# Kernel tuning notes

Hardware: AMD Instinct MI355X
Metric: run time of the kernel (lower is better)

Reference implementation:

```python
import jax, jax.numpy as jnp
import numpy as np

N = 50000
E = 800000
FEAT, COND, HID, LAT = 64, 32, 64, 32


def gcn_conv(x, W, b, src, dst, n):
    xw = x @ W  # [N, out]
    deg = jnp.zeros((n,), xw.dtype).at[dst].add(1.0) + 1.0  # in-degree + self loop
    dinv = jax.lax.rsqrt(deg)
    coef = dinv[src] * dinv[dst]  # [E]
    msg = xw[src] * coef[:, None]  # gather + scale
    agg = jax.ops.segment_sum(msg, dst, num_segments=n)
    agg = agg + xw * (1.0 / deg)[:, None]  # self-loop contribution
    return agg + b


def setup_inputs() -> dict:
    key = jax.random.key(0)
    ks = jax.random.split(key, 12)
    s = 0.05
    return {
        "feature": jax.random.normal(ks[0], (N, FEAT), jnp.float32),
        "condition": jax.random.normal(ks[1], (N, COND), jnp.float32),
        "edge_index": jax.random.randint(ks[2], (2, E), 0, N, jnp.int64),
        "enc_i2h_W": jax.random.normal(ks[3], (FEAT + COND, HID), jnp.float32) * s,
        "enc_i2h_b": jnp.zeros((HID,), jnp.float32),
        "enc_mean_W": jax.random.normal(ks[4], (HID, LAT), jnp.float32) * s,
        "enc_mean_b": jnp.zeros((LAT,), jnp.float32),
        "enc_logvar_W": jax.random.normal(ks[5], (HID, LAT), jnp.float32) * s,
        "enc_logvar_b": jnp.zeros((LAT,), jnp.float32),
        "dec_i2h_W": jax.random.normal(ks[6], (LAT + COND, HID), jnp.float32) * s,
        "dec_i2h_b": jnp.zeros((HID,), jnp.float32),
        "dec_out_W": jax.random.normal(ks[7], (HID, FEAT), jnp.float32) * s,
        "dec_out_b": jnp.zeros((FEAT,), jnp.float32),
    }


def reference(feature, condition, edge_index,
              enc_i2h_W, enc_i2h_b, enc_mean_W, enc_mean_b,
              enc_logvar_W, enc_logvar_b,
              dec_i2h_W, dec_i2h_b, dec_out_W, dec_out_b):
    src, dst = edge_index[0], edge_index[1]
    n = feature.shape[0]
    # encoder
    x = jnp.concatenate([feature, condition], axis=1)
    h = jax.nn.relu(gcn_conv(x, enc_i2h_W, enc_i2h_b, src, dst, n))
    mean = gcn_conv(h, enc_mean_W, enc_mean_b, src, dst, n)
    logvar = gcn_conv(h, enc_logvar_W, enc_logvar_b, src, dst, n)
    noise = jax.random.normal(jax.random.key(42), logvar.shape, logvar.dtype)
    z = noise * jnp.exp(0.5 * logvar) + mean
    # decoder
    xd = jnp.concatenate([z, condition], axis=1)
    hd = jax.nn.relu(gcn_conv(xd, dec_i2h_W, dec_i2h_b, src, dst, n))
    out = gcn_conv(hd, dec_out_W, dec_out_b, src, dst, n)
    return (z, mean, logvar, out)
```

## Files before the change

### kernel.cpp

```cpp
#include <hip/hip_runtime.h>
#include <hip/hip_bf16.h>
#include <hip/hip_fp16.h>
#include <math.h>

typedef _Float16 f16;
typedef __attribute__((ext_vector_type(8))) _Float16 f16x8;
typedef __attribute__((ext_vector_type(4))) float f32x4;


static __device__ __forceinline__ unsigned rotl32(unsigned x, int d) {
  return (x << d) | (x >> (32 - d));
}

static __device__ __forceinline__ void threefry_0_42(unsigned& x0, unsigned& x1) {
  const unsigned ks0 = 0u, ks1 = 42u, ks2 = 0u ^ 42u ^ 0x1BD11BDAu;
  x0 += ks0; x1 += ks1;
#define TF_R(r) { x0 += x1; x1 = rotl32(x1, (r)); x1 ^= x0; }
  TF_R(13) TF_R(15) TF_R(26) TF_R(6)
  x0 += ks1; x1 += ks2 + 1u;
  TF_R(17) TF_R(29) TF_R(16) TF_R(24)
  x0 += ks2; x1 += ks0 + 2u;
  TF_R(13) TF_R(15) TF_R(26) TF_R(6)
  x0 += ks0; x1 += ks1 + 3u;
  TF_R(17) TF_R(29) TF_R(16) TF_R(24)
  x0 += ks1; x1 += ks2 + 4u;
  TF_R(13) TF_R(15) TF_R(26) TF_R(6)
  x0 += ks2; x1 += ks0 + 5u;
#undef TF_R
}

static __device__ __forceinline__ float erfinv_f(float u) {
  float w = -logf((1.0f - u) * (1.0f + u));
  float p;
  if (w < 5.0f) {
    w = w - 2.5f;
    p = 2.81022636e-08f;
    p = fmaf(p, w, 3.43273939e-07f);
    p = fmaf(p, w, -3.5233877e-06f);
    p = fmaf(p, w, -4.39150654e-06f);
    p = fmaf(p, w, 0.00021858087f);
    p = fmaf(p, w, -0.00125372503f);
    p = fmaf(p, w, -0.00417768164f);
    p = fmaf(p, w, 0.246640727f);
    p = fmaf(p, w, 1.50140941f);
  } else {
    w = sqrtf(w) - 3.0f;
    p = -0.000200214257f;
    p = fmaf(p, w, 0.000100950558f);
    p = fmaf(p, w, 0.00134934322f);
    p = fmaf(p, w, -0.00367342844f);
    p = fmaf(p, w, 0.00573950773f);
    p = fmaf(p, w, -0.0076224613f);
    p = fmaf(p, w, 0.00943887047f);
    p = fmaf(p, w, 1.00167406f);
    p = fmaf(p, w, 2.83297682f);
  }
  return p * u;
}

static __device__ __forceinline__ float jax_normal_at(unsigned j) {
  unsigned x0 = 0u, x1 = j;
  threefry_0_42(x0, x1);
  unsigned bits = x0 ^ x1;
  float f = __uint_as_float((bits >> 9) | 0x3f800000u) - 1.0f;
  float u = fmaf(f, 1.99999994f, -0.99999994f);
  return 1.41421356237f * erfinv_f(u);
}


__global__ void degree_i_kernel(const int* __restrict__ dstI, int* __restrict__ cnt, int ne) {
  int e = blockIdx.x * blockDim.x + threadIdx.x;
  if (e < ne) atomicAdd(&cnt[dstI[e]], 1);
}

__global__ __launch_bounds__(256) void bsum_kernel(const int* __restrict__ cnt,
                                                   int* __restrict__ bh, int n) {
  __shared__ int s[256];
  int i = blockIdx.x * 256 + threadIdx.x;
  s[threadIdx.x] = (i < n) ? cnt[i] : 0;
  __syncthreads();
  for (int off = 128; off > 0; off >>= 1) {
    if (threadIdx.x < off) s[threadIdx.x] += s[threadIdx.x + off];
    __syncthreads();
  }
  if (threadIdx.x == 0) bh[blockIdx.x] = s[0];
}

__global__ __launch_bounds__(256) void scanN_kernel(const int* __restrict__ cnt,
                                                    const int* __restrict__ bh,
                                                    int* __restrict__ rowptr,
                                                    float* __restrict__ dinv,
                                                    int* __restrict__ bcur,
                                                    int n, int ne, int nbuck) {
  __shared__ int sb[256];
  __shared__ int sc[256];
  __shared__ int basesh;
  const int t = threadIdx.x;
  const int b = blockIdx.x;
  sb[t] = (t < nbuck) ? bh[t] : 0;
  __syncthreads();
  for (int off = 1; off < 256; off <<= 1) {
    int x = (t >= off) ? sb[t - off] : 0;
    __syncthreads();
    sb[t] += x;
    __syncthreads();
  }
  if (t == 0) basesh = (b > 0) ? sb[b - 1] : 0;
  __syncthreads();

  int i = b * 256 + t;
  int v = (i < n) ? cnt[i] : 0;
  sc[t] = v;
  __syncthreads();
  for (int off = 1; off < 256; off <<= 1) {
    int x = (t >= off) ? sc[t - off] : 0;
    __syncthreads();
    sc[t] += x;
    __syncthreads();
  }
  const int base = basesh;
  if (i < n) {
    rowptr[i] = base + sc[t] - v;
    dinv[i] = 1.0f / sqrtf((float)v + 1.0f);
  }
  if (t == 0) bcur[b] = base;
  if (b == nbuck - 1 && t == 255) rowptr[n] = ne;
}

#define EPB 2048
__global__ __launch_bounds__(256) void fillA_kernel(
    const int* __restrict__ srcI, const int* __restrict__ dstI,
    int* __restrict__ bcur, unsigned* __restrict__ coarse, int ne) {
  __shared__ int hist[256], hpre[256], hcur[256], gbase[256];
  __shared__ unsigned st[EPB];
  const int tid = threadIdx.x;
  const int base = blockIdx.x * EPB;

  hist[tid] = 0; hcur[tid] = 0;
  __syncthreads();

  int s[8], d[8];
#pragma unroll
  for (int k = 0; k < 8; ++k) {
    int e = base + k * 256 + tid;
    if (e < ne) { s[k] = srcI[e]; d[k] = dstI[e]; }
    else        { s[k] = -1;      d[k] = 0; }
  }
#pragma unroll
  for (int k = 0; k < 8; ++k)
    if (s[k] >= 0) atomicAdd(&hist[d[k] >> 8], 1);
  __syncthreads();

  int hv = hist[tid];
  hpre[tid] = hv;
  __syncthreads();
  for (int off = 1; off < 256; off <<= 1) {
    int x = (tid >= off) ? hpre[tid - off] : 0;
    __syncthreads();
    hpre[tid] += x;
    __syncthreads();
  }

#pragma unroll
  for (int k = 0; k < 8; ++k) {
    if (s[k] >= 0) {
      int b = d[k] >> 8;
      int pos = (hpre[b] - hist[b]) + atomicAdd(&hcur[b], 1);
      st[pos] = ((unsigned)b << 24) | ((unsigned)(d[k] & 255) << 16) | (unsigned)s[k];
    }
  }
  if (hist[tid] > 0) gbase[tid] = atomicAdd(&bcur[tid], hist[tid]);
  __syncthreads();

  int cntE = ne - base; if (cntE > EPB) cntE = EPB;
  for (int i = tid; i < cntE; i += 256) {
    unsigned v = st[i];
    int b = v >> 24;
    int excl = hpre[b] - hist[b];
    coarse[gbase[b] + (i - excl)] = v & 0x00FFFFFFu;
  }
}

__global__ __launch_bounds__(256) void fillB_kernel(
    const unsigned* __restrict__ coarse, const int* __restrict__ rowptr,
    unsigned short* __restrict__ ssrc, int n, int ne) {
  __shared__ int rcur[256];
  const int b = blockIdx.x;
  const int r0 = b << 8;
  const int tid = threadIdx.x;
  if (r0 + tid < n) rcur[tid] = rowptr[r0 + tid];
  const int e0 = rowptr[r0];
  const int e1 = (r0 + 256 <= n) ? rowptr[r0 + 256] : ne;
  __syncthreads();
  for (int e = e0 + tid; e < e1; e += 256) {
    unsigned v = coarse[e];
    int r = (v >> 16) & 255;
    int pos = atomicAdd(&rcur[r], 1);
    ssrc[pos] = (unsigned short)(v & 0xFFFFu);
  }
}

template<int IN1, int IN2, bool X1HALF, bool DUALW>
__global__ __launch_bounds__(256) void gemm_mfma_kernel(
    const void* __restrict__ X1v, const float* __restrict__ X2,
    const float* __restrict__ Wa, const float* __restrict__ Wb,
    const float* __restrict__ dinv, __half* __restrict__ Y, int n) {
  constexpr int IN = IN1 + IN2;
  constexpr int IP = IN + 8;
  __shared__ f16 xs[128 * IP];
  __shared__ f16 wt[64 * IP];

  const int tid = threadIdx.x;
  const int base = blockIdx.x * 128;

  for (int i = tid; i < IN * 64; i += 256) {
    int k = i >> 6, c = i & 63;
    float w;
    if (DUALW) w = (c < 32) ? Wa[k * 32 + c] : Wb[k * 32 + (c - 32)];
    else       w = Wa[i];
    wt[c * IP + k] = (f16)w;
  }
  if (X1HALF) {
    const __half* X1 = (const __half*)X1v;
    for (int idx = tid; idx < 128 * (IN1 / 8); idx += 256) {
      int node = idx / (IN1 / 8);
      int k8 = (idx % (IN1 / 8)) * 8;
      int g = base + node;
      f16x8 v = {};
      if (g < n) v = *(const f16x8*)(X1 + (size_t)g * IN1 + k8);
      *(f16x8*)&xs[node * IP + k8] = v;
    }
  } else {
    const float* X1 = (const float*)X1v;
    for (int idx = tid; idx < 128 * (IN1 / 4); idx += 256) {
      int node = idx / (IN1 / 4);
      int k4 = (idx % (IN1 / 4)) * 4;
      int g = base + node;
      float4 v = (g < n) ? *(const float4*)(X1 + (size_t)g * IN1 + k4)
                         : make_float4(0.f, 0.f, 0.f, 0.f);
      f16* p = &xs[node * IP + k4];
      p[0] = (f16)v.x; p[1] = (f16)v.y; p[2] = (f16)v.z; p[3] = (f16)v.w;
    }
  }
  if (IN2 > 0) {
    for (int idx = tid; idx < 128 * (IN2 / 4); idx += 256) {
      int node = idx / (IN2 / 4);
      int k4 = (idx % (IN2 / 4)) * 4;
      int g = base + node;
      float4 v = (g < n) ? *(const float4*)(X2 + (size_t)g * IN2 + k4)
                         : make_float4(0.f, 0.f, 0.f, 0.f);
      f16* p = &xs[node * IP + IN1 + k4];
      p[0] = (f16)v.x; p[1] = (f16)v.y; p[2] = (f16)v.z; p[3] = (f16)v.w;
    }
  }
  __syncthreads();

  const int wid  = tid >> 6;
  const int lane = tid & 63;
  const int l15  = lane & 15;
  const int lk8  = (lane >> 4) * 8;

  f32x4 acc[2][4] = {{{0.f,0.f,0.f,0.f}}};
  constexpr int KB = IN / 32;
#pragma unroll
  for (int kb = 0; kb < KB; ++kb) {
    const int k0 = kb * 32 + lk8;
    f16x8 a0 = *(const f16x8*)&xs[(wid * 32 +      l15) * IP + k0];
    f16x8 a1 = *(const f16x8*)&xs[(wid * 32 + 16 + l15) * IP + k0];
#pragma unroll
    for (int ct = 0; ct < 4; ++ct) {
      f16x8 b = *(const f16x8*)&wt[(ct * 16 + l15) * IP + k0];
      acc[0][ct] = __builtin_amdgcn_mfma_f32_16x16x32_f16(a0, b, acc[0][ct], 0, 0, 0);
      acc[1][ct] = __builtin_amdgcn_mfma_f32_16x16x32_f16(a1, b, acc[1][ct], 0, 0, 0);
    }
  }

#pragma unroll
  for (int rt = 0; rt < 2; ++rt) {
#pragma unroll
    for (int i = 0; i < 4; ++i) {
      int node = base + wid * 32 + rt * 16 + (lane >> 4) * 4 + i;
      if (node < n) {
        float dv = dinv[node];
#pragma unroll
        for (int ct = 0; ct < 4; ++ct) {
          Y[(size_t)node * 64 + ct * 16 + l15] = __float2half(acc[rt][ct][i] * dv);
        }
      }
    }
  }
}

template<int MODE>
__global__ __launch_bounds__(256) void gather_kernel(
    const int* __restrict__ rowptr, const unsigned short* __restrict__ ssrc,
    const __half* __restrict__ xwp, const float* __restrict__ dinv,
    const float* __restrict__ b0, const float* __restrict__ b1,
    void* __restrict__ outv, int n) {
  const int node = (blockIdx.x * 256 + threadIdx.x) >> 6;
  const int lane = threadIdx.x & 63;
  if (node >= n) return;
  const int hf = lane >> 5;
  const int cl = lane & 31;

  float2 a1, a2, a3, a4;
  a2.x = a2.y = a3.x = a3.y = a4.x = a4.y = 0.f;
  {
    float2 f = __half22float2(((const __half2*)(xwp + (size_t)node * 64))[cl]);
    a1.x = hf ? 0.f : f.x;
    a1.y = hf ? 0.f : f.y;
  }

  const int beg = rowptr[node];
  const int end = rowptr[node + 1];
  for (int cbase = beg; cbase < end; cbase += 64) {
    int m = end - cbase; if (m > 64) m = 64;
    unsigned sv = (lane < m) ? (unsigned)ssrc[cbase + lane] : 0u;
    int k = 0;
    for (; k + 7 < m; k += 8) {
      unsigned sa = __shfl(sv, k + 0 + hf, 64);
      unsigned sb = __shfl(sv, k + 2 + hf, 64);
      unsigned sc = __shfl(sv, k + 4 + hf, 64);
      unsigned sd = __shfl(sv, k + 6 + hf, 64);
      float2 fa = __half22float2(((const __half2*)(xwp + (size_t)sa * 64))[cl]);
      float2 fb = __half22float2(((const __half2*)(xwp + (size_t)sb * 64))[cl]);
      float2 fc = __half22float2(((const __half2*)(xwp + (size_t)sc * 64))[cl]);
      float2 fd = __half22float2(((const __half2*)(xwp + (size_t)sd * 64))[cl]);
      a1.x += fa.x; a1.y += fa.y;
      a2.x += fb.x; a2.y += fb.y;
      a3.x += fc.x; a3.y += fc.y;
      a4.x += fd.x; a4.y += fd.y;
    }
    for (; k + 1 < m; k += 2) {
      unsigned sa = __shfl(sv, k + hf, 64);
      float2 fa = __half22float2(((const __half2*)(xwp + (size_t)sa * 64))[cl]);
      a1.x += fa.x; a1.y += fa.y;
    }
    if (k < m) {
      unsigned sa = __shfl(sv, k, 64);
      if (hf == 0) {
        float2 fa = __half22float2(((const __half2*)(xwp + (size_t)sa * 64))[cl]);
        a1.x += fa.x; a1.y += fa.y;
      }
    }
  }
  float2 acc;
  acc.x = (a1.x + a2.x) + (a3.x + a4.x);
  acc.y = (a1.y + a2.y) + (a3.y + a4.y);
  acc.x += __shfl(acc.x, lane ^ 32, 64);
  acc.y += __shfl(acc.y, lane ^ 32, 64);
  float dv = dinv[node];
  float vx = acc.x * dv, vy = acc.y * dv;

  if (hf != 0) return;

  const int c0 = 2 * cl;
  if (MODE == 0) {
    __half* out = (__half*)outv;
    __half2 o = __floats2half2_rn(fmaxf(vx + b0[c0], 0.0f), fmaxf(vy + b0[c0 + 1], 0.0f));
    ((__half2*)(out + (size_t)node * 64))[cl] = o;
  } else if (MODE == 2) {
    float* out = (float*)outv;
    float2 o;
    o.x = vx + b0[c0];
    o.y = vy + b0[c0 + 1];
    ((float2*)(out + (size_t)node * 64))[cl] = o;
  } else {
    float* out = (float*)outv;
    float bx = (c0 < 32) ? b0[c0] : b1[c0 - 32];
    float by = (c0 + 1 < 32) ? b0[c0 + 1] : b1[c0 + 1 - 32];
    vx += bx; vy += by;
    float ox = __shfl(vx, lane + 16, 64);
    float oy = __shfl(vy, lane + 16, 64);
    const int NZ = n * 32;
    if (cl < 16) {
      int j = node * 32 + c0;
      float n0 = jax_normal_at((unsigned)j);
      float n1 = jax_normal_at((unsigned)(j + 1));
      out[j]     = fmaf(n0, expf(0.5f * ox), vx);
      out[j + 1] = fmaf(n1, expf(0.5f * oy), vy);
      out[NZ + j]     = vx;
      out[NZ + j + 1] = vy;
    } else {
      int j = node * 32 + (c0 - 32);
      out[2 * NZ + j]     = vx;
      out[2 * NZ + j + 1] = vy;
    }
  }
}


extern "C" void kernel_launch(void* const* d_in, const int* in_sizes, int n_in,
                              void* d_out, int out_size, void* d_ws, size_t ws_size,
                              hipStream_t stream) {
  const float* feat = (const float*)d_in[0];
  const float* cond = (const float*)d_in[1];
  const int*   eidx = (const int*)d_in[2];
  const float* W1  = (const float*)d_in[3];
  const float* b1  = (const float*)d_in[4];
  const float* Wm  = (const float*)d_in[5];
  const float* bm  = (const float*)d_in[6];
  const float* Wlv = (const float*)d_in[7];
  const float* blv = (const float*)d_in[8];
  const float* Wd  = (const float*)d_in[9];
  const float* bd  = (const float*)d_in[10];
  const float* Wo  = (const float*)d_in[11];
  const float* bo  = (const float*)d_in[12];

  const int n  = in_sizes[0] / 64;
  const int ne = in_sizes[2] / 2;
  const int* srcI = eidx;
  const int* dstI = eidx + ne;
  const int nbuck = (n + 255) >> 8;

  int*   cnt    = (int*)d_ws;
  int*   rowptr = cnt + n;
  int*   bh     = rowptr + n + 1;
  int*   bcur   = bh + 256;
  float* dinv   = (float*)(bcur + 256 + 3);
  __half* xwp   = (__half*)(dinv + n);
  __half* h     = xwp + (size_t)n * 64;
  unsigned short* ssrc = (unsigned short*)(h + (size_t)n * 64);
  unsigned* coarse = (unsigned*)(ssrc + ne + (ne & 1));

  float* dout   = (float*)d_out;
  float* zbuf   = dout;
  float* outbuf = dout + (size_t)3 * n * 32;

  const int BT = 256;
  auto blk = [](long long t) { return (int)((t + 255) / 256); };
  const int nb_e  = blk(ne);
  const int nb_gw = blk((long long)n * 64);
  const int nb_g  = (n + 127) / 128;
  const int nb_fa = (ne + EPB - 1) / EPB;

  hipMemsetAsync(cnt, 0, (size_t)n * sizeof(int), stream);
  hipLaunchKernelGGL(degree_i_kernel, dim3(nb_e), dim3(BT), 0, stream, dstI, cnt, ne);
  hipLaunchKernelGGL(bsum_kernel, dim3(nbuck), dim3(BT), 0, stream, cnt, bh, n);
  hipLaunchKernelGGL(scanN_kernel, dim3(nbuck), dim3(BT), 0, stream,
                     cnt, bh, rowptr, dinv, bcur, n, ne, nbuck);
  hipLaunchKernelGGL(fillA_kernel, dim3(nb_fa), dim3(BT), 0, stream, srcI, dstI, bcur, coarse, ne);
  hipLaunchKernelGGL(fillB_kernel, dim3(nbuck), dim3(BT), 0, stream, coarse, rowptr, ssrc, n, ne);

  hipLaunchKernelGGL((gemm_mfma_kernel<64, 32, false, false>), dim3(nb_g), dim3(BT), 0, stream,
                     feat, cond, W1, nullptr, dinv, xwp, n);
  hipLaunchKernelGGL((gather_kernel<0>), dim3(nb_gw), dim3(BT), 0, stream,
                     rowptr, ssrc, xwp, dinv, b1, nullptr, h, n);

  hipLaunchKernelGGL((gemm_mfma_kernel<64, 0, true, true>), dim3(nb_g), dim3(BT), 0, stream,
                     h, nullptr, Wm, Wlv, dinv, xwp, n);
  hipLaunchKernelGGL((gather_kernel<1>), dim3(nb_gw), dim3(BT), 0, stream,
                     rowptr, ssrc, xwp, dinv, bm, blv, dout, n);

  hipLaunchKernelGGL((gemm_mfma_kernel<32, 32, false, false>), dim3(nb_g), dim3(BT), 0, stream,
                     zbuf, cond, Wd, nullptr, dinv, xwp, n);
  hipLaunchKernelGGL((gather_kernel<0>), dim3(nb_gw), dim3(BT), 0, stream,
                     rowptr, ssrc, xwp, dinv, bd, nullptr, h, n);

  hipLaunchKernelGGL((gemm_mfma_kernel<64, 0, true, false>), dim3(nb_g), dim3(BT), 0, stream,
                     h, nullptr, Wo, nullptr, dinv, xwp, n);
  hipLaunchKernelGGL((gather_kernel<2>), dim3(nb_gw), dim3(BT), 0, stream,
                     rowptr, ssrc, xwp, dinv, bo, nullptr, outbuf, n);
}
```

Before: 231.2 us.

## Partially sort CSR neighbor lists by source quarter for gather locality

Measured after the change: 227.9 us (median of 2 runs). Within noise of the previous version (-1.4%).

```diff
diff --git a/kernel.cpp b/kernel.cpp
--- a/kernel.cpp
+++ b/kernel.cpp
@@ -6,6 +6,9 @@
 typedef _Float16 f16;
 typedef __attribute__((ext_vector_type(8))) _Float16 f16x8;
 typedef __attribute__((ext_vector_type(4))) float f32x4;
+
+#define NQ 4
+#define QDIV 12500
 
 
 static __device__ __forceinline__ unsigned rotl32(unsigned x, int d) {
@@ -68,16 +71,25 @@
 }
 
 
-__global__ void degree_i_kernel(const int* __restrict__ dstI, int* __restrict__ cnt, int ne) {
+__global__ void degree_i_kernel(const int* __restrict__ srcI, const int* __restrict__ dstI,
+                                int* __restrict__ cntQ, int ne) {
   int e = blockIdx.x * blockDim.x + threadIdx.x;
-  if (e < ne) atomicAdd(&cnt[dstI[e]], 1);
-}
-
-__global__ __launch_bounds__(256) void bsum_kernel(const int* __restrict__ cnt,
+  if (e < ne) {
+    int s = srcI[e], d = dstI[e];
+    atomicAdd(&cntQ[d * NQ + s / QDIV], 1);
+  }
+}
+
+__global__ __launch_bounds__(256) void bsum_kernel(const int* __restrict__ cntQ,
                                                    int* __restrict__ bh, int n) {
   __shared__ int s[256];
-  int i = blockIdx.x * 256 + threadIdx.x;
-  s[threadIdx.x] = (i < n) ? cnt[i] : 0;
+  int i4 = blockIdx.x * 1024 + threadIdx.x * 4;
+  int v = 0;
+  if (i4 < n * NQ) {
+    int4 q = *(const int4*)(cntQ + i4);
+    v = q.x + q.y + q.z + q.w;
+  }
+  s[threadIdx.x] = v;
   __syncthreads();
   for (int off = 128; off > 0; off >>= 1) {
     if (threadIdx.x < off) s[threadIdx.x] += s[threadIdx.x + off];
@@ -86,7 +98,7 @@
   if (threadIdx.x == 0) bh[blockIdx.x] = s[0];
 }
 
-__global__ __launch_bounds__(256) void scanN_kernel(const int* __restrict__ cnt,
+__global__ __launch_bounds__(256) void scanN_kernel(const int* __restrict__ cntQ,
                                                     const int* __restrict__ bh,
                                                     int* __restrict__ rowptr,
                                                     float* __restrict__ dinv,
@@ -109,7 +121,11 @@
   __syncthreads();
 
   int i = b * 256 + t;
-  int v = (i < n) ? cnt[i] : 0;
+  int v = 0;
+  if (i < n) {
+    int4 q = *(const int4*)(cntQ + i * NQ);
+    v = q.x + q.y + q.z + q.w;
+  }
   sc[t] = v;
   __syncthreads();
   for (int off = 1; off < 256; off <<= 1) {
@@ -183,20 +199,29 @@
 
 __global__ __launch_bounds__(256) void fillB_kernel(
     const unsigned* __restrict__ coarse, const int* __restrict__ rowptr,
-    unsigned short* __restrict__ ssrc, int n, int ne) {
-  __shared__ int rcur[256];
+    const int* __restrict__ cntQ, unsigned short* __restrict__ ssrc, int n, int ne) {
+  __shared__ int rcur[NQ * 256];
   const int b = blockIdx.x;
   const int r0 = b << 8;
   const int tid = threadIdx.x;
-  if (r0 + tid < n) rcur[tid] = rowptr[r0 + tid];
+  if (r0 + tid < n) {
+    int c = rowptr[r0 + tid];
+    int4 q = *(const int4*)(cntQ + (r0 + tid) * NQ);
+    rcur[0 * 256 + tid] = c;
+    rcur[1 * 256 + tid] = c + q.x;
+    rcur[2 * 256 + tid] = c + q.x + q.y;
+    rcur[3 * 256 + tid] = c + q.x + q.y + q.z;
+  }
   const int e0 = rowptr[r0];
   const int e1 = (r0 + 256 <= n) ? rowptr[r0 + 256] : ne;
   __syncthreads();
   for (int e = e0 + tid; e < e1; e += 256) {
     unsigned v = coarse[e];
     int r = (v >> 16) & 255;
-    int pos = atomicAdd(&rcur[r], 1);
-    ssrc[pos] = (unsigned short)(v & 0xFFFFu);
+    int s = v & 0xFFFFu;
+    int q = s / QDIV;
+    int pos = atomicAdd(&rcur[q * 256 + r], 1);
+    ssrc[pos] = (unsigned short)s;
   }
 }
 
@@ -413,8 +438,8 @@
   const int* dstI = eidx + ne;
   const int nbuck = (n + 255) >> 8;
 
-  int*   cnt    = (int*)d_ws;
-  int*   rowptr = cnt + n;
+  int*   cntQ   = (int*)d_ws;
+  int*   rowptr = cntQ + (size_t)n * NQ;
   int*   bh     = rowptr + n + 1;
   int*   bcur   = bh + 256;
   float* dinv   = (float*)(bcur + 256 + 3);
@@ -434,13 +459,13 @@
   const int nb_g  = (n + 127) / 128;
   const int nb_fa = (ne + EPB - 1) / EPB;
 
-  hipMemsetAsync(cnt, 0, (size_t)n * sizeof(int), stream);
-  hipLaunchKernelGGL(degree_i_kernel, dim3(nb_e), dim3(BT), 0, stream, dstI, cnt, ne);
-  hipLaunchKernelGGL(bsum_kernel, dim3(nbuck), dim3(BT), 0, stream, cnt, bh, n);
+  hipMemsetAsync(cntQ, 0, (size_t)n * NQ * sizeof(int), stream);
+  hipLaunchKernelGGL(degree_i_kernel, dim3(nb_e), dim3(BT), 0, stream, srcI, dstI, cntQ, ne);
+  hipLaunchKernelGGL(bsum_kernel, dim3(nbuck), dim3(BT), 0, stream, cntQ, bh, n);
   hipLaunchKernelGGL(scanN_kernel, dim3(nbuck), dim3(BT), 0, stream,
-                     cnt, bh, rowptr, dinv, bcur, n, ne, nbuck);
+                     cntQ, bh, rowptr, dinv, bcur, n, ne, nbuck);
   hipLaunchKernelGGL(fillA_kernel, dim3(nb_fa), dim3(BT), 0, stream, srcI, dstI, bcur, coarse, ne);
-  hipLaunchKernelGGL(fillB_kernel, dim3(nbuck), dim3(BT), 0, stream, coarse, rowptr, ssrc, n, ne);
+  hipLaunchKernelGGL(fillB_kernel, dim3(nbuck), dim3(BT), 0, stream, coarse, rowptr, cntQ, ssrc, n, ne);
 
   hipLaunchKernelGGL((gemm_mfma_kernel<64, 32, false, false>), dim3(nb_g), dim3(BT), 0, stream,
                      feat, cond, W1, nullptr, dinv, xwp, n);
```
